# Kernel optimization log

Hardware: AMD Instinct MI355X
Metric: run time of the kernel (lower is better)

The kernel has to match this reference:

```python
import jax, jax.numpy as jnp
import numpy as np

B, S, H, D, M = 8, 1024, 16, 64, 1024


def setup_inputs() -> dict:
    key = jax.random.key(0)
    ks = jax.random.split(key, 7)
    return {
        "query_tensor": jax.random.normal(ks[0], (B, S, H, D), dtype=jnp.float32),
        "key_tensor": jax.random.normal(ks[1], (B, S, H, D), dtype=jnp.float32),
        "value_tensor": jax.random.normal(ks[2], (B, H, S, D), dtype=jnp.float32),
        "qm_b": jax.random.randint(ks[3], (M,), 0, B, dtype=jnp.int32),
        "qm_s": jax.random.randint(ks[4], (M,), 0, S, dtype=jnp.int32),
        "km_b": jax.random.randint(ks[5], (M,), 0, B, dtype=jnp.int32),
        "km_s": jax.random.randint(ks[6], (M,), 0, S, dtype=jnp.int32),
    }


def reference(query_tensor, key_tensor, value_tensor, qm_b, qm_s, km_b, km_s):
    b, s, h, d = query_tensor.shape
    scale = 1.0 / jnp.sqrt(jnp.asarray(d, jnp.float32))
    # (B,H,Sq,Sk) = Q K^T / sqrt(d); q,k given as (B,S,H,D)
    corr = jnp.einsum('bqhd,bkhd->bhqk', query_tensor, key_tensor) * scale
    # masks: query_mask zeros whole rows, key_mask zeros whole columns
    row_masked = jnp.zeros((b, s), dtype=bool).at[qm_b, qm_s].set(True)
    col_masked = jnp.zeros((b, s), dtype=bool).at[km_b, km_s].set(True)
    masked = row_masked[:, None, :, None] | col_masked[:, None, None, :]
    corr = jnp.where(masked, jnp.asarray(-1e10, corr.dtype), corr)
    attn = jax.nn.softmax(corr, axis=-1)
    # value_tensor is already (B,H,S,D) per the original (no permute applied)
    return jnp.einsum('bhqk,bhkd->bhqd', attn, value_tensor)
```

## Files before the change

kernel.cpp:

```cpp
#include <hip/hip_runtime.h>
#include <stdint.h>

#define GLOBAL_AS __attribute__((address_space(1)))
#define LDS_AS __attribute__((address_space(3)))

namespace {
constexpr int Bn = 8, Sn = 1024, Hn = 16, Dn = 64, Mn = 1024;
constexpr int BQ = 128;
constexpr int TK = 64;
constexpr int NT = Sn / TK;
constexpr int LDE = 72;
constexpr int TILE_SH = 2 * 64 * LDE;
constexpr size_t BLOB_BYTES = (size_t)Bn * Hn * NT * TILE_SH * 2;
constexpr size_t ROWM_OFF = BLOB_BYTES;
constexpr float kSC = 0.125f * 1.4426950408889634f;

using f32x16 = __attribute__((ext_vector_type(16))) float;
using s16x4 = __attribute__((ext_vector_type(4))) short;
using s16x8 = __attribute__((ext_vector_type(8))) short;

__device__ inline unsigned short f2bf(float f) {
    union { float f; unsigned u; } v; v.f = f;
    return (unsigned short)((v.u + 0x7FFFu + ((v.u >> 16) & 1u)) >> 16);
}
__device__ inline unsigned pk2(float a, float b) {
    return (unsigned)f2bf(a) | ((unsigned)f2bf(b) << 16);
}

#if __has_builtin(__builtin_amdgcn_exp2f)
#define EXP2F __builtin_amdgcn_exp2f
#else
#define EXP2F exp2f
#endif
}

__global__ __launch_bounds__(256) void convert2(
    const float* __restrict__ K, const float* __restrict__ V,
    unsigned short* __restrict__ blob)
{
    __shared__ float Vl[64 * 65];
    const int t = threadIdx.x;
    const int kt = blockIdx.x, h = blockIdx.y, b = blockIdx.z;
    unsigned short* out = blob + ((size_t)((b * Hn + h) * NT + kt)) * TILE_SH;

    const int key = t >> 2, dg = (t & 3) * 16;
    {
        const float* kp = K + (((size_t)b * Sn + kt * TK + key) * Hn + h) * Dn + dg;
        uint2 w[4];
        #pragma unroll
        for (int j = 0; j < 4; ++j) {
            float4 v = *(const float4*)(kp + j * 4);
            w[j].x = pk2(v.x, v.y); w[j].y = pk2(v.z, v.w);
        }
        uint2* o = (uint2*)&out[key * LDE + dg];
        #pragma unroll
        for (int j = 0; j < 4; ++j) o[j] = w[j];
    }
    {
        const float* vp = V + (((size_t)b * Hn + h) * Sn + kt * TK + key) * Dn + dg;
        #pragma unroll
        for (int j = 0; j < 4; ++j) {
            float4 v = *(const float4*)(vp + j * 4);
            Vl[(dg + j * 4 + 0) * 65 + key] = v.x;
            Vl[(dg + j * 4 + 1) * 65 + key] = v.y;
            Vl[(dg + j * 4 + 2) * 65 + key] = v.z;
            Vl[(dg + j * 4 + 3) * 65 + key] = v.w;
        }
    }
    __syncthreads();
    {
        const int d = t >> 2, kc = (t & 3) * 16;
        float tmp[16];
        #pragma unroll
        for (int i = 0; i < 16; ++i) tmp[i] = Vl[d * 65 + kc + i];
        uint2* o = (uint2*)&out[64 * LDE + d * LDE + kc];
        #pragma unroll
        for (int j = 0; j < 4; ++j) {
            uint2 w; w.x = pk2(tmp[j * 4 + 0], tmp[j * 4 + 1]);
            w.y = pk2(tmp[j * 4 + 2], tmp[j * 4 + 3]);
            o[j] = w;
        }
    }
}

__global__ __launch_bounds__(1024) void masks_k(
    const int* __restrict__ qmb, const int* __restrict__ qms,
    const int* __restrict__ kmb, const int* __restrict__ kms,
    unsigned int* __restrict__ wsm)
{
    const int t = threadIdx.x;
    wsm[t] = 0; wsm[t + 1024] = 0;
    if (t < 256) wsm[t + 2048] = 0;
    __syncthreads();
    unsigned char* rowm = (unsigned char*)wsm;
    unsigned long long* colbits = (unsigned long long*)(wsm + 2048);
    rowm[qmb[t] * Sn + qms[t]] = 1;
    atomicOr(&colbits[kmb[t] * NT + (kms[t] >> 6)], 1ull << (kms[t] & 63));
}

__global__ __launch_bounds__(128, 2) void attn2(
    const float* __restrict__ Q, const unsigned short* __restrict__ blob,
    const unsigned char* __restrict__ rowm,
    const unsigned long long* __restrict__ colbits,
    float* __restrict__ Out)
{
    __shared__ unsigned short KV[TILE_SH];
    __shared__ float Ls[2][2][32];
    const int t = threadIdx.x;
    const int wave = t >> 6, lane = t & 63;
    const int l31 = lane & 31, q2 = lane >> 5;
    const int bh = blockIdx.x, b = bh >> 4, h = bh & 15;
    const int qb = blockIdx.y * BQ + wave * 64;

    s16x8 qf[2][4];
    float rmONE[2];
    unsigned rmKEEP[2];
    #pragma unroll
    for (int sub = 0; sub < 2; ++sub) {
        const float* qp = Q + (((size_t)b * Sn + qb + sub * 32 + l31) * Hn + h) * Dn + q2 * 8;
        #pragma unroll
        for (int st = 0; st < 4; ++st) {
            float4 a = *(const float4*)(qp + st * 16);
            float4 c = *(const float4*)(qp + st * 16 + 4);
            s16x8 f;
            f[0] = (short)f2bf(a.x * kSC); f[1] = (short)f2bf(a.y * kSC);
            f[2] = (short)f2bf(a.z * kSC); f[3] = (short)f2bf(a.w * kSC);
            f[4] = (short)f2bf(c.x * kSC); f[5] = (short)f2bf(c.y * kSC);
            f[6] = (short)f2bf(c.z * kSC); f[7] = (short)f2bf(c.w * kSC);
            qf[sub][st] = f;
        }
        const bool rmb = rowm[b * Sn + qb + sub * 32 + l31] != 0;
        rmONE[sub] = rmb ? 1.0f : 0.0f;
        rmKEEP[sub] = rmb ? 0u : 0xFFFFFFFFu;
    }

    f32x16 O[2][2];
    #pragma unroll
    for (int sub = 0; sub < 2; ++sub)
        #pragma unroll
        for (int dt = 0; dt < 2; ++dt)
            #pragma unroll
            for (int i = 0; i < 16; ++i) O[sub][dt][i] = 0.0f;
    float lsum[2] = {0.0f, 0.0f};

    const unsigned short* tile0 = blob + (size_t)bh * NT * TILE_SH;

    for (int kt = 0; kt < NT; ++kt) {
        __syncthreads();
        {
            const GLOBAL_AS unsigned int* g =
                (const GLOBAL_AS unsigned int*)(tile0 + (size_t)kt * TILE_SH);
            LDS_AS unsigned int* l = (LDS_AS unsigned int*)KV;
            #pragma unroll
            for (int j = 0; j < 9; ++j)
                __builtin_amdgcn_global_load_lds(g + (j * 2048 + t * 16) / 4,
                                                 l + (j * 2048 + t * 16) / 4, 16, 0, 0);
        }
        const unsigned long long cmask = colbits[b * NT + kt];
        __syncthreads();

        #pragma unroll
        for (int ct = 0; ct < 2; ++ct) {
            s16x8 kf[4];
            #pragma unroll
            for (int st = 0; st < 4; ++st)
                kf[st] = *(const s16x8*)&KV[(ct * 32 + l31) * LDE + st * 16 + q2 * 8];
            const unsigned ncm = ~(((unsigned)(cmask >> (ct * 32))) >> (q2 * 4));

            s16x8 P[2][2];
            #pragma unroll
            for (int sub = 0; sub < 2; ++sub) {
                f32x16 sc;
                #pragma unroll
                for (int i = 0; i < 16; ++i) sc[i] = 0.0f;
                #pragma unroll
                for (int st = 0; st < 4; ++st)
                    sc = __builtin_amdgcn_mfma_f32_32x32x16_bf16(kf[st], qf[sub][st], sc, 0, 0, 0);
                const unsigned keep = ncm & rmKEEP[sub];
                unsigned u[8];
                #pragma unroll
                for (int c = 0; c < 4; ++c) {
                    float p[4];
                    #pragma unroll
                    for (int j = 0; j < 4; ++j) {
                        float e = EXP2F(sc[4 * c + j]);
                        e = ((keep >> (8 * c + j)) & 1u) ? e : 0.0f;
                        p[j] = e + rmONE[sub];
                    }
                    lsum[sub] += (p[0] + p[1]) + (p[2] + p[3]);
                    u[2 * c]     = pk2(p[0], p[1]);
                    u[2 * c + 1] = pk2(p[2], p[3]);
                }
                union { unsigned w[4]; s16x8 v; } f0, f1;
                f0.w[0] = u[0]; f0.w[1] = u[1]; f0.w[2] = u[2]; f0.w[3] = u[3];
                f1.w[0] = u[4]; f1.w[1] = u[5]; f1.w[2] = u[6]; f1.w[3] = u[7];
                P[sub][0] = f0.v;
                P[sub][1] = f1.v;
            }
            #pragma unroll
            for (int dt = 0; dt < 2; ++dt)
                #pragma unroll
                for (int ch = 0; ch < 2; ++ch) {
                    const int base = 64 * LDE + (dt * 32 + l31) * LDE + ct * 32 + ch * 16 + q2 * 4;
                    s16x4 lo = *(const s16x4*)&KV[base];
                    s16x4 hi = *(const s16x4*)&KV[base + 8];
                    s16x8 vf = __builtin_shufflevector(lo, hi, 0, 1, 2, 3, 4, 5, 6, 7);
                    O[0][dt] = __builtin_amdgcn_mfma_f32_32x32x16_bf16(P[0][ch], vf, O[0][dt], 0, 0, 0);
                    O[1][dt] = __builtin_amdgcn_mfma_f32_32x32x16_bf16(P[1][ch], vf, O[1][dt], 0, 0, 0);
                }
        }
    }

    #pragma unroll
    for (int sub = 0; sub < 2; ++sub) {
        float s = lsum[sub] + __shfl_xor(lsum[sub], 32, 64);
        if (lane < 32) Ls[wave][sub][l31] = 1.0f / s;
    }
    __syncthreads();
    float* op = Out + ((size_t)(b * Hn + h)) * Sn * Dn;
    #pragma unroll
    for (int sub = 0; sub < 2; ++sub)
        #pragma unroll
        for (int reg = 0; reg < 16; ++reg) {
            const int qrow = (reg & 3) + 8 * (reg >> 2) + 4 * q2;
            const float invl = Ls[wave][sub][qrow];
            const int q = qb + sub * 32 + qrow;
            #pragma unroll
            for (int dt = 0; dt < 2; ++dt)
                op[(size_t)q * Dn + dt * 32 + l31] = O[sub][dt][reg] * invl;
        }
}

extern "C" void kernel_launch(void* const* d_in, const int* in_sizes, int n_in,
                              void* d_out, int out_size, void* d_ws, size_t ws_size,
                              hipStream_t stream) {
    (void)in_sizes; (void)n_in; (void)out_size; (void)ws_size;
    const float* Q = (const float*)d_in[0];
    const float* K = (const float*)d_in[1];
    const float* V = (const float*)d_in[2];
    const int* qmb = (const int*)d_in[3];
    const int* qms = (const int*)d_in[4];
    const int* kmb = (const int*)d_in[5];
    const int* kms = (const int*)d_in[6];
    float* Out = (float*)d_out;

    unsigned short* blob = (unsigned short*)d_ws;
    unsigned int* wsm = (unsigned int*)(void*)((char*)d_ws + ROWM_OFF);
    const unsigned char* rowm = (const unsigned char*)wsm;
    const unsigned long long* colbits = (const unsigned long long*)(wsm + 2048);

    masks_k<<<1, 1024, 0, stream>>>(qmb, qms, kmb, kms, wsm);
    convert2<<<dim3(NT, Hn, Bn), 256, 0, stream>>>(K, V, blob);
    attn2<<<dim3(Bn * Hn, Sn / BQ), 128, 0, stream>>>(Q, blob, rowm, colbits, Out);
}
```

Before: 207.7 us.

## Double-buffer K/V tiles in LDS and use native bf16 conversion

The K/V tile for step kt+1 is now prefetched into a second LDS buffer while step kt is computed, with the first tile loaded in a prologue before the Q conversion. This drops one barrier per iteration and is meant to hide global-to-LDS load latency behind the MFMA work. The manual round-to-nearest bf16 packing is replaced by the compiler's __bf16 casts, and the mask select becomes a bitfield-extract AND. The cmask global load is issued after the prefetch, so an in-order vmcnt wait could still serialise on the prefetch and reduce the overlap. LDS use per block doubles.

```diff
diff --git a/kernel.cpp b/kernel.cpp
--- a/kernel.cpp
+++ b/kernel.cpp
@@ -19,12 +19,10 @@
 using s16x4 = __attribute__((ext_vector_type(4))) short;
 using s16x8 = __attribute__((ext_vector_type(8))) short;
 
-__device__ inline unsigned short f2bf(float f) {
-    union { float f; unsigned u; } v; v.f = f;
-    return (unsigned short)((v.u + 0x7FFFu + ((v.u >> 16) & 1u)) >> 16);
-}
 __device__ inline unsigned pk2(float a, float b) {
-    return (unsigned)f2bf(a) | ((unsigned)f2bf(b) << 16);
+    union { __bf16 h[2]; unsigned u; } x;
+    x.h[0] = (__bf16)a; x.h[1] = (__bf16)b;
+    return x.u;
 }
 
 #if __has_builtin(__builtin_amdgcn_exp2f)
@@ -98,13 +96,13 @@
     atomicOr(&colbits[kmb[t] * NT + (kms[t] >> 6)], 1ull << (kms[t] & 63));
 }
 
-__global__ __launch_bounds__(128, 2) void attn2(
+__global__ __launch_bounds__(128, 2) void attn3(
     const float* __restrict__ Q, const unsigned short* __restrict__ blob,
     const unsigned char* __restrict__ rowm,
     const unsigned long long* __restrict__ colbits,
     float* __restrict__ Out)
 {
-    __shared__ unsigned short KV[TILE_SH];
+    __shared__ unsigned short KV2[2][TILE_SH];
     __shared__ float Ls[2][2][32];
     const int t = threadIdx.x;
     const int wave = t >> 6, lane = t & 63;
@@ -112,6 +110,17 @@
     const int bh = blockIdx.x, b = bh >> 4, h = bh & 15;
     const int qb = blockIdx.y * BQ + wave * 64;
 
+    const unsigned short* tile0 = blob + (size_t)bh * NT * TILE_SH;
+
+    {
+        const GLOBAL_AS unsigned int* g = (const GLOBAL_AS unsigned int*)tile0;
+        LDS_AS unsigned int* l = (LDS_AS unsigned int*)&KV2[0][0];
+        #pragma unroll
+        for (int j = 0; j < 9; ++j)
+            __builtin_amdgcn_global_load_lds(g + (j * 2048 + t * 16) / 4,
+                                             l + (j * 2048 + t * 16) / 4, 16, 0, 0);
+    }
+
     s16x8 qf[2][4];
     float rmONE[2];
     unsigned rmKEEP[2];
@@ -122,12 +131,12 @@
         for (int st = 0; st < 4; ++st) {
             float4 a = *(const float4*)(qp + st * 16);
             float4 c = *(const float4*)(qp + st * 16 + 4);
-            s16x8 f;
-            f[0] = (short)f2bf(a.x * kSC); f[1] = (short)f2bf(a.y * kSC);
-            f[2] = (short)f2bf(a.z * kSC); f[3] = (short)f2bf(a.w * kSC);
-            f[4] = (short)f2bf(c.x * kSC); f[5] = (short)f2bf(c.y * kSC);
-            f[6] = (short)f2bf(c.z * kSC); f[7] = (short)f2bf(c.w * kSC);
-            qf[sub][st] = f;
+            union { unsigned w[4]; s16x8 v; } f;
+            f.w[0] = pk2(a.x * kSC, a.y * kSC);
+            f.w[1] = pk2(a.z * kSC, a.w * kSC);
+            f.w[2] = pk2(c.x * kSC, c.y * kSC);
+            f.w[3] = pk2(c.z * kSC, c.w * kSC);
+            qf[sub][st] = f.v;
         }
         const bool rmb = rowm[b * Sn + qb + sub * 32 + l31] != 0;
         rmONE[sub] = rmb ? 1.0f : 0.0f;
@@ -143,28 +152,28 @@
             for (int i = 0; i < 16; ++i) O[sub][dt][i] = 0.0f;
     float lsum[2] = {0.0f, 0.0f};
 
-    const unsigned short* tile0 = blob + (size_t)bh * NT * TILE_SH;
-
     for (int kt = 0; kt < NT; ++kt) {
+        const int cur = kt & 1;
         __syncthreads();
-        {
+        if (kt + 1 < NT) {
             const GLOBAL_AS unsigned int* g =
-                (const GLOBAL_AS unsigned int*)(tile0 + (size_t)kt * TILE_SH);
-            LDS_AS unsigned int* l = (LDS_AS unsigned int*)KV;
+                (const GLOBAL_AS unsigned int*)(tile0 + (size_t)(kt + 1) * TILE_SH);
+            LDS_AS unsigned int* l = (LDS_AS unsigned int*)&KV2[cur ^ 1][0];
             #pragma unroll
             for (int j = 0; j < 9; ++j)
                 __builtin_amdgcn_global_load_lds(g + (j * 2048 + t * 16) / 4,
                                                  l + (j * 2048 + t * 16) / 4, 16, 0, 0);
         }
+        const unsigned short* Kl = &KV2[cur][0];
+        const unsigned short* Vt = &KV2[cur][64 * LDE];
         const unsigned long long cmask = colbits[b * NT + kt];
-        __syncthreads();
 
         #pragma unroll
         for (int ct = 0; ct < 2; ++ct) {
             s16x8 kf[4];
             #pragma unroll
             for (int st = 0; st < 4; ++st)
-                kf[st] = *(const s16x8*)&KV[(ct * 32 + l31) * LDE + st * 16 + q2 * 8];
+                kf[st] = *(const s16x8*)&Kl[(ct * 32 + l31) * LDE + st * 16 + q2 * 8];
             const unsigned ncm = ~(((unsigned)(cmask >> (ct * 32))) >> (q2 * 4));
 
             s16x8 P[2][2];
@@ -184,8 +193,8 @@
                     #pragma unroll
                     for (int j = 0; j < 4; ++j) {
                         float e = EXP2F(sc[4 * c + j]);
-                        e = ((keep >> (8 * c + j)) & 1u) ? e : 0.0f;
-                        p[j] = e + rmONE[sub];
+                        unsigned m = (unsigned)__builtin_amdgcn_sbfe((int)keep, 8 * c + j, 1);
+                        p[j] = __uint_as_float(__float_as_uint(e) & m) + rmONE[sub];
                     }
                     lsum[sub] += (p[0] + p[1]) + (p[2] + p[3]);
                     u[2 * c]     = pk2(p[0], p[1]);
@@ -201,9 +210,9 @@
             for (int dt = 0; dt < 2; ++dt)
                 #pragma unroll
                 for (int ch = 0; ch < 2; ++ch) {
-                    const int base = 64 * LDE + (dt * 32 + l31) * LDE + ct * 32 + ch * 16 + q2 * 4;
-                    s16x4 lo = *(const s16x4*)&KV[base];
-                    s16x4 hi = *(const s16x4*)&KV[base + 8];
+                    const int base = (dt * 32 + l31) * LDE + ct * 32 + ch * 16 + q2 * 4;
+                    s16x4 lo = *(const s16x4*)&Vt[base];
+                    s16x4 hi = *(const s16x4*)&Vt[base + 8];
                     s16x8 vf = __builtin_shufflevector(lo, hi, 0, 1, 2, 3, 4, 5, 6, 7);
                     O[0][dt] = __builtin_amdgcn_mfma_f32_32x32x16_bf16(P[0][ch], vf, O[0][dt], 0, 0, 0);
                     O[1][dt] = __builtin_amdgcn_mfma_f32_32x32x16_bf16(P[1][ch], vf, O[1][dt], 0, 0, 0);
@@ -251,5 +260,5 @@
 
     masks_k<<<1, 1024, 0, stream>>>(qmb, qms, kmb, kms, wsm);
     convert2<<<dim3(NT, Hn, Bn), 256, 0, stream>>>(K, V, blob);
-    attn2<<<dim3(Bn * Hn, Sn / BQ), 128, 0, stream>>>(Q, blob, rowm, colbits, Out);
-}
+    attn3<<<dim3(Bn * Hn, Sn / BQ), 128, 0, stream>>>(Q, blob, rowm, colbits, Out);
+}
```

After: 264.1 us. +27.2%, slower.
